# Optimization experiments

Measured on AMD Instinct MI355X. Metric: run time of the kernel, lower is better.

Reference implementation:

```python
import jax, jax.numpy as jnp
import numpy as np

N = 100_000   # nodes
E = 1_600_000 # edges
D_IN = 64
HID = 512
OUT = 64
NSEG = HID // OUT  # 8
P = [0, 1, 2]
BN_EPS = 1e-5


def setup_inputs() -> dict:
    key = jax.random.key(0)
    ks = jax.random.split(key, 16)
    feats = jax.random.normal(ks[0], (N, D_IN), dtype=jnp.float32)
    src = jax.random.randint(ks[1], (E,), 0, N, dtype=jnp.int32)
    dst = jax.random.randint(ks[2], (E,), 0, N, dtype=jnp.int32)
    s_in = 1.0 / np.sqrt(D_IN)
    s_fc = 1.0 / np.sqrt(HID * len(P))
    W0 = jax.random.uniform(ks[3], (HID, D_IN), jnp.float32, -s_in, s_in)
    b0 = jnp.zeros((HID,), jnp.float32)
    W1 = jax.random.uniform(ks[4], (HID, D_IN), jnp.float32, -s_in, s_in)
    b1 = jnp.zeros((HID,), jnp.float32)
    W2 = jax.random.uniform(ks[5], (HID, D_IN), jnp.float32, -s_in, s_in)
    b2 = jnp.zeros((HID,), jnp.float32)
    fc_W = jax.random.uniform(ks[6], (HID, HID * len(P)), jnp.float32, -s_fc, s_fc)
    fc_b = jnp.zeros((HID,), jnp.float32)
    gamma = jnp.ones((HID,), jnp.float32)
    beta = jnp.zeros((HID,), jnp.float32)
    q = jax.random.uniform(ks[7], (NSEG,), jnp.float32)
    return dict(feats=feats, src=src, dst=dst, W0=W0, b0=b0, W1=W1, b1=b1,
                W2=W2, b2=b2, fc_W=fc_W, fc_b=fc_b, gamma=gamma, beta=beta, q=q)


def _mixhop_layer(feats, src, dst, Ws, bs, fc_W, fc_b, gamma, beta):
    # degree norm: deg^{-1/2}, clamped at 1
    deg = jax.ops.segment_sum(jnp.ones((E,), feats.dtype), dst, num_segments=N)
    norm = jnp.clip(deg, 1.0, None) ** -0.5  # [N]
    norm = norm[:, None]
    outputs = []
    h = feats
    for j in range(max(P) + 1):
        h = h * norm
        # SpMM: sum over incoming edges (copy_u + sum)
        h = jax.ops.segment_sum(h[src], dst, num_segments=N)
        h = h * norm
        if j in P:
            outputs.append(h @ Ws[j].T + bs[j])  # [N, HID]
    cat = jnp.concatenate(outputs, axis=1)       # [N, 3*HID]
    final = cat @ fc_W.T + fc_b                  # [N, HID]
    # BatchNorm1d (training-mode batch statistics, biased var)
    mu = jnp.mean(final, axis=0)
    var = jnp.mean((final - mu) ** 2, axis=0)
    final = (final - mu) * jax.lax.rsqrt(var + BN_EPS) * gamma + beta
    return final


def reference(feats, src, dst, W0, b0, W1, b1, W2, b2, fc_W, fc_b, gamma, beta, q):
    h = _mixhop_layer(feats, src, dst, [W0, W1, W2], [b0, b1, b2],
                      fc_W, fc_b, gamma, beta)           # [N, HID]
    # segment mixing: sum_k q[k] * h[:, k*OUT:(k+1)*OUT]
    out = jnp.einsum('nko,k->no', h.reshape(N, NSEG, OUT), q)  # [N, OUT]
    return out
```

## Files before the change

### kernel.cpp

```cpp
#include <hip/hip_runtime.h>
#include <hip/hip_bf16.h>
#include <stdint.h>

typedef unsigned short ushort;
typedef unsigned int uint;
typedef unsigned char uchar;

#define N_NODES 100000
#define N_EDGES 1600000
#define KDIM 192
#define HIDDEN 512
#define NCHUNK 782
#define SDIM (KDIM*KDIM)
#define NPAIR 78
#define PPB   9984
#define NSPLIT 8
#define LDT 194
#define NSLICE 256
#define EPS (N_EDGES/NSLICE)

#define NB 391
#define BCAP 5120

typedef __attribute__((ext_vector_type(8))) short short8;
typedef __attribute__((ext_vector_type(4))) short short4v;
typedef __attribute__((ext_vector_type(4))) uint uint4v;
typedef __attribute__((ext_vector_type(4))) float float4v;
typedef __attribute__((ext_vector_type(2))) float float2v;
typedef __attribute__((ext_vector_type(2))) uint uint2v;

__device__ __forceinline__ float bf2f(ushort u){
    uint x = ((uint)u) << 16;
    return __builtin_bit_cast(float, x);
}
__device__ __forceinline__ float bflo(uint u){
    return __builtin_bit_cast(float, u << 16);
}
__device__ __forceinline__ float bfhi(uint u){
    return __builtin_bit_cast(float, u & 0xffff0000u);
}
__device__ __forceinline__ ushort f2bf(float f){
    uint u = __builtin_bit_cast(uint, f);
    u += 0x7fffu + ((u >> 16) & 1u);
    return (ushort)(u >> 16);
}

__global__ __launch_bounds__(1024) void k_histA(const int* __restrict__ dst,
                                                uint* __restrict__ histA){
    __shared__ uint cnt[NB];
    int slice = blockIdx.x, t = threadIdx.x;
    for (int b = t; b < NB; b += 1024) cnt[b] = 0;
    __syncthreads();
    int e0 = slice * EPS;
    for (int i = t; i < EPS; i += 1024){
        uint d = (uint)dst[e0 + i];
        atomicAdd(&cnt[d >> 8], 1u);
    }
    __syncthreads();
    for (int b = t; b < NB; b += 1024) histA[(size_t)b*NSLICE + slice] = cnt[b];
}

__global__ void k_scanSl(const uint* __restrict__ histA, uint* __restrict__ sbase,
                         uint* __restrict__ btot){
    __shared__ uint sc[NSLICE];
    int b = blockIdx.x, t = threadIdx.x;
    uint v = histA[(size_t)b*NSLICE + t];
    sc[t] = v; __syncthreads();
    for (int off = 1; off < 256; off <<= 1){
        uint u = (t >= off) ? sc[t - off] : 0;
        __syncthreads();
        sc[t] += u;
        __syncthreads();
    }
    sbase[(size_t)b*NSLICE + t] = sc[t] - v;
    if (t == 255) btot[b] = sc[255];
}

__global__ void k_scanBk(const uint* __restrict__ btot, uint* __restrict__ bstart){
    __shared__ uint sc[512];
    int t = threadIdx.x;
    uint v = (t < NB) ? btot[t] : 0;
    sc[t] = v; __syncthreads();
    for (int off = 1; off < 512; off <<= 1){
        uint u = (t >= off) ? sc[t - off] : 0;
        __syncthreads();
        sc[t] += u;
        __syncthreads();
    }
    if (t < NB) bstart[t] = sc[t] - v;
}

__global__ __launch_bounds__(1024) void k_packA(const int* __restrict__ src,
                                                const int* __restrict__ dst,
                                                const uint* __restrict__ sbase,
                                                const uint* __restrict__ bstart,
                                                uint* __restrict__ rec){
    __shared__ uint arr[NB];
    int slice = blockIdx.x, t = threadIdx.x;
    for (int b = t; b < NB; b += 1024)
        arr[b] = bstart[b] + sbase[(size_t)b*NSLICE + slice];
    __syncthreads();
    int e0 = slice * EPS;
    for (int i = t; i < EPS; i += 1024){
        int e = e0 + i;
        uint d = (uint)dst[e];
        uint bk = d >> 8;
        uint slot = atomicAdd(&arr[bk], 1u);
        rec[slot] = (uint)src[e] | ((d & 255u) << 17);
    }
}

__global__ __launch_bounds__(256) void k_passB(const uint* __restrict__ rec,
                                               const uint* __restrict__ bstart,
                                               const uint* __restrict__ btot,
                                               int* __restrict__ csr,
                                               int* __restrict__ deg,
                                               int* __restrict__ rowptr,
                                               float* __restrict__ nrm){
    __shared__ uint recs[BCAP];
    __shared__ uint cntL[256];
    __shared__ uint ofs[256];
    int b = blockIdx.x, t = threadIdx.x;
    uint base = bstart[b], cnt = btot[b];
    cntL[t] = 0;
    __syncthreads();
    for (uint i = t; i < cnt; i += 256){
        uint rv = rec[base + i];
        if (i < BCAP) recs[i] = rv;
        atomicAdd(&cntL[(rv >> 17) & 255u], 1u);
    }
    __syncthreads();
    uint c = cntL[t];
    ofs[t] = c; __syncthreads();
    for (int off = 1; off < 256; off <<= 1){
        uint u = (t >= off) ? ofs[t - off] : 0;
        __syncthreads();
        ofs[t] += u;
        __syncthreads();
    }
    uint excl = ofs[t] - c;
    int node = b*256 + t;
    if (node < N_NODES){
        deg[node] = (int)c;
        rowptr[node] = (int)(base + excl);
        nrm[node] = rsqrtf((float)(c > 0 ? c : 1));
    }
    __syncthreads();
    ofs[t] = excl;
    __syncthreads();
    for (uint i = t; i < cnt; i += 256){
        uint rv = (i < BCAP) ? recs[i] : rec[base + i];
        uint n = (rv >> 17) & 255u;
        uint p = atomicAdd(&ofs[n], 1u);
        csr[base + p] = (int)(rv & 0x1FFFFu);
    }
}

__global__ void k_cast(const float* __restrict__ feats, const float* __restrict__ nrm,
                       ushort* __restrict__ Hx){
    int i = blockIdx.x * 256 + threadIdx.x;
    if (i < N_NODES * 16){
        float w = nrm[i >> 4];
        float4v v = ((const float4v*)feats)[i];
        short4v o;
        o[0] = (short)f2bf(v[0]*w); o[1] = (short)f2bf(v[1]*w);
        o[2] = (short)f2bf(v[2]*w); o[3] = (short)f2bf(v[3]*w);
        ((short4v*)Hx)[i] = o;
    }
}

template<bool WRITE_HS>
__global__ void k_agg(const ushort* __restrict__ inp,
                      ushort* __restrict__ H, int outoff,
                      ushort* __restrict__ Hs,
                      const int* __restrict__ rowptr, const int* __restrict__ deg,
                      const float* __restrict__ nrm, const int* __restrict__ csr){
    int node = (blockIdx.x << 3) + (threadIdx.x >> 5);
    int lane = threadIdx.x & 63;
    if (node >= N_NODES) return;
    int slot = (lane & 31) >> 3;
    int fb   = lane & 7;
    int beg = rowptr[node];
    int d   = deg[node];
    float acc[8] = {};
    int i = 0;
    for (; i + 8 <= d; i += 8){
        int sA = csr[beg + i + slot];
        int sB = csr[beg + i + 4 + slot];
        uint4v vA = *(const uint4v*)(inp + (long)sA*64 + fb*8);
        uint4v vB = *(const uint4v*)(inp + (long)sB*64 + fb*8);
        #pragma unroll
        for (int p = 0; p < 4; ++p){
            acc[2*p]   += bflo(vA[p]); acc[2*p+1] += bfhi(vA[p]);
            acc[2*p]   += bflo(vB[p]); acc[2*p+1] += bfhi(vB[p]);
        }
    }
    if (i + 4 <= d){
        int sA = csr[beg + i + slot];
        uint4v vA = *(const uint4v*)(inp + (long)sA*64 + fb*8);
        #pragma unroll
        for (int p = 0; p < 4; ++p){
            acc[2*p]   += bflo(vA[p]); acc[2*p+1] += bfhi(vA[p]);
        }
        i += 4;
    }
    if (i + slot < d){
        int s = csr[beg + i + slot];
        uint4v v = *(const uint4v*)(inp + (long)s*64 + fb*8);
        #pragma unroll
        for (int p = 0; p < 4; ++p){
            acc[2*p]   += bflo(v[p]); acc[2*p+1] += bfhi(v[p]);
        }
    }
    #pragma unroll
    for (int k = 0; k < 8; ++k){
        acc[k] += __shfl_xor(acc[k], 8);
        acc[k] += __shfl_xor(acc[k], 16);
    }
    if (slot == 0){
        float wn = nrm[node];
        short8 o;
        #pragma unroll
        for (int k = 0; k < 8; ++k) o[k] = (short)f2bf(wn * acc[k]);
        *(short8*)(H + (long)node*KDIM + outoff + fb*8) = o;
        if (WRITE_HS){
            float w2 = wn * wn;
            short8 o2;
            #pragma unroll
            for (int k = 0; k < 8; ++k) o2[k] = (short)f2bf(w2 * acc[k]);
            *(short8*)(Hs + (long)node*64 + fb*8) = o2;
        }
    }
}

__global__ __launch_bounds__(192) void k_prepM1(const float* __restrict__ W0,
                                                const float* __restrict__ W1,
                                                const float* __restrict__ W2,
                                                const float* __restrict__ fcW,
                                                float* __restrict__ MTp){
    int ks = blockIdx.x;
    int c0 = blockIdx.y * 4;
    int jd = threadIdx.x;
    int j = jd >> 6, d = jd & 63;
    const float* W  = (j == 0) ? W0 : (j == 1) ? W1 : W2;
    const float* wp = W + (ks*64)*64 + d;
    const float* f0 = fcW + (long)(c0+0)*1536 + j*512 + ks*64;
    const float* f1 = fcW + (long)(c0+1)*1536 + j*512 + ks*64;
    const float* f2 = fcW + (long)(c0+2)*1536 + j*512 + ks*64;
    const float* f3 = fcW + (long)(c0+3)*1536 + j*512 + ks*64;
    float a0 = 0.f, a1 = 0.f, a2 = 0.f, a3 = 0.f;
    #pragma unroll 8
    for (int k = 0; k < 64; ++k){
        float w = wp[k*64];
        a0 += w * f0[k]; a1 += w * f1[k]; a2 += w * f2[k]; a3 += w * f3[k];
    }
    long base = (long)ks*(HIDDEN*KDIM) + (long)c0*KDIM + jd;
    MTp[base]         = a0;
    MTp[base + KDIM]  = a1;
    MTp[base + 2*KDIM]= a2;
    MTp[base + 3*KDIM]= a3;
}

__global__ void k_prepM2(const float* __restrict__ MTp, ushort* __restrict__ MT){
    int i = blockIdx.x*256 + threadIdx.x;
    if (i >= HIDDEN*KDIM) return;
    float s = 0.f;
    #pragma unroll
    for (int ks = 0; ks < 8; ++ks) s += MTp[(long)ks*(HIDDEN*KDIM) + i];
    MT[i] = f2bf(s);
}

__global__ __launch_bounds__(256) void k_bias(const float* __restrict__ b0,
                                              const float* __restrict__ b1,
                                              const float* __restrict__ b2,
                                              const float* __restrict__ fcW,
                                              const float* __restrict__ fcb,
                                              float* __restrict__ Bc){
    __shared__ float red[256];
    int c = blockIdx.x, t = threadIdx.x;
    const float* fw = fcW + (long)c*1536;
    float s = b0[t]*fw[t]          + b0[t+256]*fw[t+256]
            + b1[t]*fw[512+t]      + b1[t+256]*fw[512+t+256]
            + b2[t]*fw[1024+t]     + b2[t+256]*fw[1024+t+256];
    red[t] = s; __syncthreads();
    for (int off = 128; off > 0; off >>= 1){
        if (t < off) red[t] += red[t + off];
        __syncthreads();
    }
    if (t == 0) Bc[c] = fcb[c] + red[0];
}

template<int W>
__device__ __forceinline__ void do_pairs(const short8* frag, float4v* acc){
    int p = 0, c = 0;
    #pragma unroll
    for (int i = 0; i < 12; ++i)
        #pragma unroll
        for (int j = i; j < 12; ++j){
            if ((p & 3) == W){
                acc[c] = __builtin_amdgcn_mfma_f32_16x16x32_bf16(frag[i], frag[j], acc[c], 0,0,0);
                ++c;
            }
            ++p;
        }
}
template<int W>
__device__ __forceinline__ void store_pairs(const float4v* acc, uint* Pb, int lane){
    int p = 0, c = 0;
    #pragma unroll
    for (int i = 0; i < 12; ++i)
        #pragma unroll
        for (int j = i; j < 12; ++j){
            if ((p & 3) == W){
                uint2v v;
                v[0] = (uint)f2bf(acc[c][0]) | ((uint)f2bf(acc[c][1]) << 16);
                v[1] = (uint)f2bf(acc[c][2]) | ((uint)f2bf(acc[c][3]) << 16);
                *(uint2v*)(Pb + p*128 + lane*2) = v;
                ++c;
            }
            ++p;
        }
}

__global__ __launch_bounds__(256, 2) void k_hth(const ushort* __restrict__ H,
                                                uint* __restrict__ P,
                                                float* __restrict__ msum){
    __shared__ ushort Ts[128*LDT];
    int t = threadIdx.x;
    int w = t >> 6, lane = t & 63;
    int m16 = lane & 15, quad = lane >> 4;
    int n0 = blockIdx.x * 128;
    #pragma unroll
    for (int it = 0; it < 12; ++it){
        int flat = it*256 + t;
        int row = flat / 24, seg = flat - row*24;
        int gr = n0 + row;
        short8 v = {0,0,0,0,0,0,0,0};
        if (gr < N_NODES) v = *(const short8*)(H + (long)gr*KDIM + seg*8);
        *(short8*)(Ts + row*LDT + seg*8) = v;
    }
    __syncthreads();
    float4v acc[20] = {};
    #pragma unroll
    for (int kt = 0; kt < 4; ++kt){
        short8 frag[12];
        #pragma unroll
        for (int b = 0; b < 12; ++b){
            short8 f;
            #pragma unroll
            for (int j = 0; j < 8; ++j)
                f[j] = (short)Ts[(kt*32 + quad*8 + j)*LDT + b*16 + m16];
            frag[b] = f;
        }
        if      (w == 0) do_pairs<0>(frag, acc);
        else if (w == 1) do_pairs<1>(frag, acc);
        else if (w == 2) do_pairs<2>(frag, acc);
        else             do_pairs<3>(frag, acc);
    }
    if (t < KDIM){
        float s = 0.f;
        #pragma unroll 4
        for (int n = 0; n < 128; ++n) s += bf2f(Ts[n*LDT + t]);
        atomicAdd(&msum[t], s);
    }
    uint* Pb = P + (long)blockIdx.x * PPB;
    if      (w == 0) store_pairs<0>(acc, Pb, lane);
    else if (w == 1) store_pairs<1>(acc, Pb, lane);
    else if (w == 2) store_pairs<2>(acc, Pb, lane);
    else             store_pairs<3>(acc, Pb, lane);
}

__global__ void k_reduce(const uint* __restrict__ P, float* __restrict__ SP){
    int p = blockIdx.x * 256 + threadIdx.x;
    int y = blockIdx.y;
    int b0 = y * 98, b1 = min(b0 + 98, NCHUNK);
    float lo = 0.f, hi = 0.f;
    for (int b = b0; b < b1; ++b){
        uint v = P[(long)b*PPB + p];
        lo += bf2f((ushort)(v & 0xffff));
        hi += bf2f((ushort)(v >> 16));
    }
    float2v o; o[0] = lo; o[1] = hi;
    *(float2v*)(SP + (long)y*(NPAIR*256) + p*2) = o;
}

__global__ void k_finC(const float* __restrict__ SP, const float* __restrict__ msum,
                       float* __restrict__ C){
    int idx = blockIdx.x * 256 + threadIdx.x;
    float s = 0.f;
    #pragma unroll
    for (int y = 0; y < NSPLIT; ++y) s += SP[(long)y*(NPAIR*256) + idx];
    int h = idx & 1, pu = idx >> 1;
    int p = pu >> 7, rem = pu & 127;
    int l = rem >> 1, u = rem & 1;
    int r = u*2 + h;
    int pi = 0, pj = 0, off = 0;
    #pragma unroll
    for (int k = 0; k < 12; ++k){
        int len = 12 - k;
        if (p >= off && p < off + len){ pi = k; pj = k + (p - off); }
        off += len;
    }
    int m = pi*16 + (l >> 4)*4 + r;
    int n = pj*16 + (l & 15);
    const float invN = 1.f / (float)N_NODES;
    float v = s*invN - (msum[m]*invN)*(msum[n]*invN);
    C[m*KDIM + n] = v;
    C[n*KDIM + m] = v;
}

__global__ void k_cv(const float* __restrict__ C, const ushort* __restrict__ MT,
                     float* __restrict__ V){
    int c = blockIdx.x, d = threadIdx.x;
    const ushort* mt = MT + c*KDIM;
    float s = 0.f;
    #pragma unroll 4
    for (int dp = 0; dp < KDIM; ++dp)
        s += bf2f(mt[dp]) * C[dp*KDIM + d];
    V[c*KDIM + d] = s;
}

__global__ void k_solve2(const float* __restrict__ V, const ushort* __restrict__ MT,
                         const float* __restrict__ msum, const float* __restrict__ Bc,
                         const float* __restrict__ gamma, const float* __restrict__ beta,
                         const float* __restrict__ q,
                         float* __restrict__ rr, float* __restrict__ cvec){
    __shared__ float tmp[HIDDEN];
    int c = threadIdx.x;
    const float invN = 1.f / (float)N_NODES;
    float mu = Bc[c], var = 0.f;
    const ushort* mt = MT + c*KDIM;
    const float* vc = V + c*KDIM;
    #pragma unroll 4
    for (int d = 0; d < KDIM; ++d){
        float m = bf2f(mt[d]);
        mu  += msum[d]*invN * m;
        var += vc[d] * m;
    }
    float r = gamma[c] * rsqrtf(var + 1e-5f);
    rr[c] = r;
    tmp[c] = r * (Bc[c] - mu) + beta[c];
    __syncthreads();
    if (c < 64){
        float s = 0.f;
        #pragma unroll
        for (int k = 0; k < 8; ++k) s += q[k] * tmp[k*64 + c];
        cvec[c] = s;
    }
}

__global__ void k_buildG(const ushort* __restrict__ MT, const float* __restrict__ rr,
                         const float* __restrict__ q, ushort* __restrict__ GT){
    int o = blockIdx.x, d = threadIdx.x;
    float s = 0.f;
    #pragma unroll
    for (int k = 0; k < 8; ++k)
        s += q[k] * rr[k*64 + o] * bf2f(MT[(k*64 + o)*KDIM + d]);
    GT[o*KDIM + d] = f2bf(s);
}

#define LDA 200
__global__ __launch_bounds__(256) void k_outgemm(const ushort* __restrict__ H,
                                                 const ushort* __restrict__ GT,
                                                 const float* __restrict__ cvec,
                                                 float* __restrict__ out){
    __shared__ ushort As[128*LDA];
    __shared__ ushort Gs[64*LDA];
    int t = threadIdx.x;
    int n0 = blockIdx.x * 128;
    int w = t >> 6, lane = t & 63;
    int m16 = lane & 15, quad = lane >> 4;
    int wr = w * 32;
    float4v acc[2][4] = {};
    #pragma unroll
    for (int it = 0; it < 12; ++it){
        int flat = it*256 + t;
        int row = flat / 24, seg = flat - row*24;
        int gr = n0 + row;
        short8 v = {0,0,0,0,0,0,0,0};
        if (gr < N_NODES) v = *(const short8*)(H + (long)gr*KDIM + seg*8);
        *(short8*)(As + row*LDA + seg*8) = v;
    }
    #pragma unroll
    for (int it = 0; it < 6; ++it){
        int flat = it*256 + t;
        int row = flat / 24, seg = flat - row*24;
        short8 v = *(const short8*)(GT + row*KDIM + seg*8);
        *(short8*)(Gs + row*LDA + seg*8) = v;
    }
    __syncthreads();
    #pragma unroll
    for (int kk = 0; kk < 192; kk += 32){
        short8 af[2], bf[4];
        #pragma unroll
        for (int i = 0; i < 2; ++i)
            af[i] = *(const short8*)(As + (wr + i*16 + m16)*LDA + kk + quad*8);
        #pragma unroll
        for (int j = 0; j < 4; ++j)
            bf[j] = *(const short8*)(Gs + (j*16 + m16)*LDA + kk + quad*8);
        #pragma unroll
        for (int i = 0; i < 2; ++i)
            #pragma unroll
            for (int j = 0; j < 4; ++j)
                acc[i][j] = __builtin_amdgcn_mfma_f32_16x16x32_bf16(af[i], bf[j], acc[i][j], 0,0,0);
    }
    #pragma unroll
    for (int i = 0; i < 2; ++i)
        #pragma unroll
        for (int j = 0; j < 4; ++j)
            #pragma unroll
            for (int r = 0; r < 4; ++r){
                int rowg = n0 + wr + i*16 + quad*4 + r;
                int o = j*16 + m16;
                if (rowg < N_NODES) out[(long)rowg*64 + o] = acc[i][j][r] + cvec[o];
            }
}

extern "C" void kernel_launch(void* const* d_in, const int* in_sizes, int n_in,
                              void* d_out, int out_size, void* d_ws, size_t ws_size,
                              hipStream_t stream) {
    const float* feats = (const float*)d_in[0];
    const int*   src   = (const int*)  d_in[1];
    const int*   dst   = (const int*)  d_in[2];
    const float* W0    = (const float*)d_in[3];
    const float* b0    = (const float*)d_in[4];
    const float* W1    = (const float*)d_in[5];
    const float* b1    = (const float*)d_in[6];
    const float* W2    = (const float*)d_in[7];
    const float* b2    = (const float*)d_in[8];
    const float* fcW   = (const float*)d_in[9];
    const float* fcb   = (const float*)d_in[10];
    const float* gamma = (const float*)d_in[11];
    const float* beta  = (const float*)d_in[12];
    const float* q     = (const float*)d_in[13];
    float* out = (float*)d_out;

    char* ws = (char*)d_ws;
    size_t off = 0;
    auto alloc = [&](size_t bytes) -> char* {
        char* p = ws + off;
        off = (off + bytes + 511) & ~(size_t)511;
        return p;
    };
    uint*   histA   = (uint*)  alloc((size_t)NB * NSLICE * 4);
    uint*   sbase   = (uint*)  alloc((size_t)NB * NSLICE * 4);
    uint*   btot    = (uint*)  alloc((size_t)NB * 4);
    uint*   bstart  = (uint*)  alloc((size_t)NB * 4);
    uint*   rec     = (uint*)  alloc((size_t)N_EDGES * 4);
    int*    deg     = (int*)   alloc((size_t)N_NODES * 4);
    int*    rowptr  = (int*)   alloc((size_t)N_NODES * 4);
    float*  nrm     = (float*) alloc((size_t)N_NODES * 4);
    int*    csr     = (int*)   alloc((size_t)N_EDGES * 4);
    ushort* Hx      = (ushort*)alloc((size_t)N_NODES * 64 * 2);
    ushort* HsB     = (ushort*)alloc((size_t)N_NODES * 64 * 2);
    ushort* H       = (ushort*)alloc((size_t)N_NODES * KDIM * 2);
    ushort* MT      = (ushort*)alloc((size_t)HIDDEN * KDIM * 2);
    float*  MTp     = (float*) alloc((size_t)8 * HIDDEN * KDIM * 4);
    float*  Bc      = (float*) alloc((size_t)HIDDEN * 4);
    float*  msum    = (float*) alloc((size_t)KDIM * 4);
    uint*   P       = (uint*)  alloc((size_t)NCHUNK * PPB * 4);
    float*  SP      = (float*) alloc((size_t)NSPLIT * NPAIR * 256 * 4);
    float*  C       = (float*) alloc((size_t)SDIM * 4);
    float*  V       = (float*) alloc((size_t)HIDDEN * KDIM * 4);
    float*  rr      = (float*) alloc((size_t)HIDDEN * 4);
    float*  cvec    = (float*) alloc((size_t)64 * 4);
    ushort* GT      = (ushort*)alloc((size_t)64 * KDIM * 2);
    (void)ws_size; (void)n_in; (void)in_sizes; (void)out_size;

    hipMemsetAsync(msum, 0, (size_t)KDIM * 4, stream);

    k_histA <<<NSLICE, 1024, 0, stream>>>(dst, histA);
    k_scanSl<<<NB, 256, 0, stream>>>(histA, sbase, btot);
    k_scanBk<<<1, 512, 0, stream>>>(btot, bstart);
    k_packA <<<NSLICE, 1024, 0, stream>>>(src, dst, sbase, bstart, rec);
    k_passB <<<NB, 256, 0, stream>>>(rec, bstart, btot, csr, deg, rowptr, nrm);

    k_cast  <<<(N_NODES*16 + 255)/256, 256, 0, stream>>>(feats, nrm, Hx);

    int aggGrid = (N_NODES + 7) / 8;
    k_agg<true> <<<aggGrid, 256, 0, stream>>>(Hx,  H, 0,   HsB, rowptr, deg, nrm, csr);
    k_agg<true> <<<aggGrid, 256, 0, stream>>>(HsB, H, 64,  Hx,  rowptr, deg, nrm, csr);
    k_agg<false><<<aggGrid, 256, 0, stream>>>(Hx,  H, 128, HsB, rowptr, deg, nrm, csr);

    dim3 pmGrid(8, HIDDEN/4);
    k_prepM1<<<pmGrid, 192, 0, stream>>>(W0, W1, W2, fcW, MTp);
    k_prepM2<<<(HIDDEN*KDIM + 255)/256, 256, 0, stream>>>(MTp, MT);
    k_bias <<<HIDDEN, 256, 0, stream>>>(b0, b1, b2, fcW, fcb, Bc);

    k_hth   <<<NCHUNK, 256, 0, stream>>>(H, P, msum);
    dim3 rGrid(PPB/256, NSPLIT);
    k_reduce<<<rGrid, 256, 0, stream>>>(P, SP);
    k_finC  <<<NPAIR, 256, 0, stream>>>(SP, msum, C);
    k_cv    <<<HIDDEN, KDIM, 0, stream>>>(C, MT, V);
    k_solve2<<<1, HIDDEN, 0, stream>>>(V, MT, msum, Bc, gamma, beta, q, rr, cvec);
    k_buildG<<<64, KDIM, 0, stream>>>(MT, rr, q, GT);

    k_outgemm<<<NCHUNK, 256, 0, stream>>>(H, GT, cvec, out);
}
```

Measured before the change: 401.7 us.

## Batch H^T H chunks per block and parallelize covariance solve kernels

k_hth now has each block loop over four 128-row chunks, accumulating in registers before writing one partial, so the partial buffer and the k_reduce pass shrink by about four times. The single-block k_solve2 becomes a split-K k_cv1, a per-channel parallel-reduction k_solveA and a small k_solveB, spreading the serial per-channel dot products across many blocks. The cost is fewer k_hth blocks (196) on the device, which lowers occupancy, plus one extra kernel launch.

```diff
diff --git a/kernel.cpp b/kernel.cpp
--- a/kernel.cpp
+++ b/kernel.cpp
@@ -11,6 +11,8 @@
 #define KDIM 192
 #define HIDDEN 512
 #define NCHUNK 782
+#define NCH 4
+#define NPART 196
 #define SDIM (KDIM*KDIM)
 #define NPAIR 78
 #define PPB   9984
@@ -329,39 +331,44 @@
     int t = threadIdx.x;
     int w = t >> 6, lane = t & 63;
     int m16 = lane & 15, quad = lane >> 4;
-    int n0 = blockIdx.x * 128;
-    #pragma unroll
-    for (int it = 0; it < 12; ++it){
-        int flat = it*256 + t;
-        int row = flat / 24, seg = flat - row*24;
-        int gr = n0 + row;
-        short8 v = {0,0,0,0,0,0,0,0};
-        if (gr < N_NODES) v = *(const short8*)(H + (long)gr*KDIM + seg*8);
-        *(short8*)(Ts + row*LDT + seg*8) = v;
-    }
-    __syncthreads();
     float4v acc[20] = {};
-    #pragma unroll
-    for (int kt = 0; kt < 4; ++kt){
-        short8 frag[12];
-        #pragma unroll
-        for (int b = 0; b < 12; ++b){
-            short8 f;
+    for (int cc = 0; cc < NCH; ++cc){
+        int chunk = blockIdx.x * NCH + cc;
+        if (chunk >= NCHUNK) break;
+        int n0 = chunk * 128;
+        #pragma unroll
+        for (int it = 0; it < 12; ++it){
+            int flat = it*256 + t;
+            int row = flat / 24, seg = flat - row*24;
+            int gr = n0 + row;
+            short8 v = {0,0,0,0,0,0,0,0};
+            if (gr < N_NODES) v = *(const short8*)(H + (long)gr*KDIM + seg*8);
+            *(short8*)(Ts + row*LDT + seg*8) = v;
+        }
+        __syncthreads();
+        #pragma unroll
+        for (int kt = 0; kt < 4; ++kt){
+            short8 frag[12];
             #pragma unroll
-            for (int j = 0; j < 8; ++j)
-                f[j] = (short)Ts[(kt*32 + quad*8 + j)*LDT + b*16 + m16];
-            frag[b] = f;
-        }
-        if      (w == 0) do_pairs<0>(frag, acc);
-        else if (w == 1) do_pairs<1>(frag, acc);
-        else if (w == 2) do_pairs<2>(frag, acc);
-        else             do_pairs<3>(frag, acc);
-    }
-    if (t < KDIM){
-        float s = 0.f;
-        #pragma unroll 4
-        for (int n = 0; n < 128; ++n) s += bf2f(Ts[n*LDT + t]);
-        atomicAdd(&msum[t], s);
+            for (int b = 0; b < 12; ++b){
+                short8 f;
+                #pragma unroll
+                for (int j = 0; j < 8; ++j)
+                    f[j] = (short)Ts[(kt*32 + quad*8 + j)*LDT + b*16 + m16];
+                frag[b] = f;
+            }
+            if      (w == 0) do_pairs<0>(frag, acc);
+            else if (w == 1) do_pairs<1>(frag, acc);
+            else if (w == 2) do_pairs<2>(frag, acc);
+            else             do_pairs<3>(frag, acc);
+        }
+        if (t < KDIM){
+            float s = 0.f;
+            #pragma unroll 4
+            for (int n = 0; n < 128; ++n) s += bf2f(Ts[n*LDT + t]);
+            atomicAdd(&msum[t], s);
+        }
+        __syncthreads();
     }
     uint* Pb = P + (long)blockIdx.x * PPB;
     if      (w == 0) store_pairs<0>(acc, Pb, lane);
@@ -373,7 +380,7 @@
 __global__ void k_reduce(const uint* __restrict__ P, float* __restrict__ SP){
     int p = blockIdx.x * 256 + threadIdx.x;
     int y = blockIdx.y;
-    int b0 = y * 98, b1 = min(b0 + 98, NCHUNK);
+    int b0 = y * 25, b1 = min(b0 + 25, NPART);
     float lo = 0.f, hi = 0.f;
     for (int b = b0; b < b1; ++b){
         uint v = P[(long)b*PPB + p];
@@ -409,44 +416,70 @@
     C[n*KDIM + m] = v;
 }
 
-__global__ void k_cv(const float* __restrict__ C, const ushort* __restrict__ MT,
-                     float* __restrict__ V){
+__global__ __launch_bounds__(192) void k_cv1(const float* __restrict__ C,
+                                             const ushort* __restrict__ MT,
+                                             float* __restrict__ Vp){
+    int ks = blockIdx.x;
+    int c0 = blockIdx.y * 4;
+    int d  = threadIdx.x;
+    const ushort* m0 = MT + (long)(c0+0)*KDIM + ks*48;
+    const ushort* m1 = MT + (long)(c0+1)*KDIM + ks*48;
+    const ushort* m2 = MT + (long)(c0+2)*KDIM + ks*48;
+    const ushort* m3 = MT + (long)(c0+3)*KDIM + ks*48;
+    const float* cp = C + (long)(ks*48)*KDIM + d;
+    float a0 = 0.f, a1 = 0.f, a2 = 0.f, a3 = 0.f;
+    #pragma unroll 8
+    for (int k = 0; k < 48; ++k){
+        float cv = cp[(long)k*KDIM];
+        a0 += bf2f(m0[k]) * cv; a1 += bf2f(m1[k]) * cv;
+        a2 += bf2f(m2[k]) * cv; a3 += bf2f(m3[k]) * cv;
+    }
+    long base = (long)ks*(HIDDEN*KDIM) + (long)c0*KDIM + d;
+    Vp[base]          = a0;
+    Vp[base + KDIM]   = a1;
+    Vp[base + 2*KDIM] = a2;
+    Vp[base + 3*KDIM] = a3;
+}
+
+__global__ __launch_bounds__(192) void k_solveA(const float* __restrict__ Vp,
+                                                const ushort* __restrict__ MT,
+                                                const float* __restrict__ msum,
+                                                const float* __restrict__ Bc,
+                                                const float* __restrict__ gamma,
+                                                const float* __restrict__ beta,
+                                                float* __restrict__ rr,
+                                                float* __restrict__ tmpBN){
+    __shared__ float redM[192];
+    __shared__ float redV[192];
     int c = blockIdx.x, d = threadIdx.x;
-    const ushort* mt = MT + c*KDIM;
+    const float invN = 1.f / (float)N_NODES;
+    float m = bf2f(MT[(long)c*KDIM + d]);
+    long vi = (long)c*KDIM + d;
+    float vsum = Vp[vi] + Vp[vi + HIDDEN*KDIM] + Vp[vi + 2*HIDDEN*KDIM]
+               + Vp[vi + 3*HIDDEN*KDIM];
+    redM[d] = msum[d]*invN * m;
+    redV[d] = vsum * m;
+    __syncthreads();
+    for (int off = 96; off >= 3; off >>= 1){
+        if (d < off){ redM[d] += redM[d + off]; redV[d] += redV[d + off]; }
+        __syncthreads();
+    }
+    if (d == 0){
+        float mu  = Bc[c] + redM[0] + redM[1] + redM[2];
+        float var = redV[0] + redV[1] + redV[2];
+        float r = gamma[c] * rsqrtf(var + 1e-5f);
+        rr[c] = r;
+        tmpBN[c] = r * (Bc[c] - mu) + beta[c];
+    }
+}
+
+__global__ void k_solveB(const float* __restrict__ tmpBN, const float* __restrict__ q,
+                         float* __restrict__ cvec){
+    int c = threadIdx.x;
     float s = 0.f;
-    #pragma unroll 4
-    for (int dp = 0; dp < KDIM; ++dp)
-        s += bf2f(mt[dp]) * C[dp*KDIM + d];
-    V[c*KDIM + d] = s;
-}
-
-__global__ void k_solve2(const float* __restrict__ V, const ushort* __restrict__ MT,
-                         const float* __restrict__ msum, const float* __restrict__ Bc,
-                         const float* __restrict__ gamma, const float* __restrict__ beta,
-                         const float* __restrict__ q,
-                         float* __restrict__ rr, float* __restrict__ cvec){
-    __shared__ float tmp[HIDDEN];
-    int c = threadIdx.x;
-    const float invN = 1.f / (float)N_NODES;
-    float mu = Bc[c], var = 0.f;
-    const ushort* mt = MT + c*KDIM;
-    const float* vc = V + c*KDIM;
-    #pragma unroll 4
-    for (int d = 0; d < KDIM; ++d){
-        float m = bf2f(mt[d]);
-        mu  += msum[d]*invN * m;
-        var += vc[d] * m;
-    }
-    float r = gamma[c] * rsqrtf(var + 1e-5f);
-    rr[c] = r;
-    tmp[c] = r * (Bc[c] - mu) + beta[c];
-    __syncthreads();
-    if (c < 64){
-        float s = 0.f;
-        #pragma unroll
-        for (int k = 0; k < 8; ++k) s += q[k] * tmp[k*64 + c];
-        cvec[c] = s;
-    }
+    #pragma unroll
+    for (int k = 0; k < 8; ++k) s += q[k] * tmpBN[k*64 + c];
+    cvec[c] = s;
 }
 
 __global__ void k_buildG(const ushort* __restrict__ MT, const float* __restrict__ rr,
@@ -558,11 +591,12 @@
     float*  MTp     = (float*) alloc((size_t)8 * HIDDEN * KDIM * 4);
     float*  Bc      = (float*) alloc((size_t)HIDDEN * 4);
     float*  msum    = (float*) alloc((size_t)KDIM * 4);
-    uint*   P       = (uint*)  alloc((size_t)NCHUNK * PPB * 4);
+    uint*   P       = (uint*)  alloc((size_t)NPART * PPB * 4);
     float*  SP      = (float*) alloc((size_t)NSPLIT * NPAIR * 256 * 4);
     float*  C       = (float*) alloc((size_t)SDIM * 4);
-    float*  V       = (float*) alloc((size_t)HIDDEN * KDIM * 4);
+    float*  Vp      = (float*) alloc((size_t)4 * HIDDEN * KDIM * 4);
     float*  rr      = (float*) alloc((size_t)HIDDEN * 4);
+    float*  tmpBN   = (float*) alloc((size_t)HIDDEN * 4);
     float*  cvec    = (float*) alloc((size_t)64 * 4);
     ushort* GT      = (ushort*)alloc((size_t)64 * KDIM * 2);
     (void)ws_size; (void)n_in; (void)in_sizes; (void)out_size;
@@ -587,12 +621,14 @@
     k_prepM2<<<(HIDDEN*KDIM + 255)/256, 256, 0, stream>>>(MTp, MT);
     k_bias <<<HIDDEN, 256, 0, stream>>>(b0, b1, b2, fcW, fcb, Bc);
 
-    k_hth   <<<NCHUNK, 256, 0, stream>>>(H, P, msum);
+    k_hth   <<<NPART, 256, 0, stream>>>(H, P, msum);
     dim3 rGrid(PPB/256, NSPLIT);
     k_reduce<<<rGrid, 256, 0, stream>>>(P, SP);
     k_finC  <<<NPAIR, 256, 0, stream>>>(SP, msum, C);
-    k_cv    <<<HIDDEN, KDIM, 0, stream>>>(C, MT, V);
-    k_solve2<<<1, HIDDEN, 0, stream>>>(V, MT, msum, Bc, gamma, beta, q, rr, cvec);
+    dim3 cvGrid(4, HIDDEN/4);
+    k_cv1   <<<cvGrid, 192, 0, stream>>>(C, MT, Vp);
+    k_solveA<<<HIDDEN, 192, 0, stream>>>(Vp, MT, msum, Bc, gamma, beta, rr, tmpBN);
+    k_solveB<<<1, 64, 0, stream>>>(tmpBN, q, cvec);
     k_buildG<<<64, KDIM, 0, stream>>>(MT, rr, q, GT);
 
     k_outgemm<<<NCHUNK, 256, 0, stream>>>(H, GT, cvec, out);
```

After: 353.8 us. 11.9% less time.
